# Optimization experiments

Hardware: AMD Instinct MI355X
Metric: run time of the kernel (lower is better)

The kernel has to match this reference:

```python
import jax, jax.numpy as jnp
import numpy as np

N_NODES = 20000
N_EDGES = 320000
N_GRAPHS = 32
C = 256
L = 4
IN_DIM = 739
EDGE_DIM = 2 * C + 6
LN_EPS = 1e-5


def _layernorm(x, g, b):
    mu = jnp.mean(x, axis=-1, keepdims=True)
    var = jnp.mean(jnp.square(x - mu), axis=-1, keepdims=True)
    return (x - mu) * jax.lax.rsqrt(var + LN_EPS) * g + b


def setup_inputs() -> dict:
    key = jax.random.key(0)
    ks = jax.random.split(key, 20)
    d = {}
    d["x"] = jax.random.normal(ks[0], (N_NODES, IN_DIM), jnp.float32)
    d["x_pos"] = jax.random.normal(ks[1], (N_NODES, 3), jnp.float32)
    d["edge_index"] = jax.random.randint(ks[2], (2, N_EDGES), 0, N_NODES, jnp.int32)
    d["batch"] = jnp.sort(jax.random.randint(ks[3], (N_NODES,), 0, N_GRAPHS, jnp.int32))
    s = 0.02
    d["dense_w"] = jax.random.normal(ks[4], (IN_DIM, C), jnp.float32) * s
    d["dense_b"] = jnp.zeros((C,), jnp.float32)
    d["d1_w"] = jax.random.normal(ks[5], (L, C, C), jnp.float32) * s
    d["d1_b"] = jnp.zeros((L, C), jnp.float32)
    d["ln1_g"] = jnp.ones((L, EDGE_DIM), jnp.float32)
    d["ln1_b"] = jnp.zeros((L, EDGE_DIM), jnp.float32)
    d["w1_w"] = jax.random.normal(ks[6], (L, EDGE_DIM, 4), jnp.float32) * s
    d["w1_b"] = jnp.zeros((L, 4), jnp.float32)
    d["ln2_g"] = jnp.ones((L, 4), jnp.float32)
    d["ln2_b"] = jnp.zeros((L, 4), jnp.float32)
    d["w2_w"] = jax.random.normal(ks[7], (L, 4, 1), jnp.float32) * s
    d["w2_b"] = jnp.zeros((L, 1), jnp.float32)
    d["d2_w"] = jax.random.normal(ks[8], (L, C, C), jnp.float32) * s
    d["d2_b"] = jnp.zeros((L, C), jnp.float32)
    d["head_w"] = jax.random.normal(ks[9], (C, 1), jnp.float32) * s
    d["head_b"] = jnp.zeros((1,), jnp.float32)
    return d


def reference(x, x_pos, edge_index, batch, dense_w, dense_b, d1_w, d1_b,
              ln1_g, ln1_b, w1_w, w1_b, ln2_g, ln2_b, w2_w, w2_b,
              d2_w, d2_b, head_w, head_b):
    n = x.shape[0]
    src, dst = edge_index[0], edge_index[1]
    h = x @ dense_w + dense_b  # [N, C]
    for l in range(d1_w.shape[0]):
        # message: dense1 -> GELU (dropout is identity in eval)
        m = jax.nn.gelu(h @ d1_w[l] + d1_b[l], approximate=False)  # [N, C]
        sx = m[src]                                                # [E, C]
        # edge-MLP input: [src_x, dst_x, src_pos, dst_pos]
        e = jnp.concatenate([sx, m[dst], x_pos[src], x_pos[dst]], axis=-1)  # [E, 2C+6]
        e = _layernorm(e, ln1_g[l], ln1_b[l])
        e = jax.nn.gelu(e @ w1_w[l] + w1_b[l], approximate=False)  # [E, 4]
        e = _layernorm(e, ln2_g[l], ln2_b[l])
        w = jax.nn.sigmoid(e @ w2_w[l] + w2_b[l])                  # [E, 1]
        agg = jax.ops.segment_sum(sx * w, dst, num_segments=n)     # [N, C]
        # update: dense2 -> GELU
        h = jax.nn.gelu(agg @ d2_w[l] + d2_b[l], approximate=False)
    # global mean pool over graphs
    sums = jax.ops.segment_sum(h, batch, num_segments=N_GRAPHS)           # [G, C]
    cnts = jax.ops.segment_sum(jnp.ones((n, 1), h.dtype), batch, num_segments=N_GRAPHS)
    pooled = sums / jnp.maximum(cnts, 1.0)
    return pooled @ head_w + head_b  # [G, 1]
```

## Files before the change

### kernel.cpp

```cpp
#include <hip/hip_runtime.h>
#include <math.h>

#define N_NODES 20000
#define N_EDGES 320000
#define N_GRAPHS 32
#define CDIM 256
#define IN_DIMV 739
#define KPAD_DENSE 768
#define ED_DIM 518
#define NLAYERS 4
#define LN_EPS 1e-5f
#define SCAN_BLOCKS ((N_NODES + 255) / 256)

typedef _Float16 f16x8 __attribute__((ext_vector_type(8)));
typedef _Float16 f16x4 __attribute__((ext_vector_type(4)));
typedef float f32x4 __attribute__((ext_vector_type(4)));

__device__ __forceinline__ float gelu_exact(float x) {
    return 0.5f * x * (1.f + erff(x * 0.7071067811865475f));
}

__device__ __forceinline__ void gll16(const void* g, void* l) {
    __builtin_amdgcn_global_load_lds((const __attribute__((address_space(1))) void*)g,
                                     (__attribute__((address_space(3))) void*)l, 16, 0, 0);
}

__global__ __launch_bounds__(256)
void prep_all(const float* __restrict__ ln1_g, const float* __restrict__ ln1_b,
              const float* __restrict__ w1_w, float* __restrict__ cw,
              float* __restrict__ SgSb,
              const float* __restrict__ dense_w, _Float16* __restrict__ wt_dense,
              const float* __restrict__ d1_w, const float* __restrict__ d2_w,
              _Float16* __restrict__ wt_sq, int* __restrict__ deg,
              float* __restrict__ sdot) {
    __shared__ float smem[2048 + 64];
    int b = blockIdx.x, tid = threadIdx.x;
    if (b < 79) {
        int i = b * 256 + tid;
        if (i < N_NODES) deg[i] = 0;
    } else if (b < 83) {
        int l = b - 79;
        float sg[4] = {0, 0, 0, 0}, sb[4] = {0, 0, 0, 0};
        for (int i = tid; i < ED_DIM; i += 256) {
            float g = ln1_g[l * ED_DIM + i];
            float bb = ln1_b[l * ED_DIM + i];
            float4 w = *(const float4*)&w1_w[(size_t)(l * ED_DIM + i) * 4];
            float4 c = make_float4(g * w.x, g * w.y, g * w.z, g * w.w);
            *(float4*)&cw[(size_t)(l * ED_DIM + i) * 4] = c;
            sg[0] += c.x; sg[1] += c.y; sg[2] += c.z; sg[3] += c.w;
            sb[0] += bb * w.x; sb[1] += bb * w.y; sb[2] += bb * w.z; sb[3] += bb * w.w;
        }
        for (int c = 0; c < 4; c++) { smem[tid * 8 + c] = sg[c]; smem[tid * 8 + 4 + c] = sb[c]; }
        __syncthreads();
        for (int s = 128; s > 0; s >>= 1) {
            if (tid < s)
                for (int c = 0; c < 8; c++) smem[tid * 8 + c] += smem[(tid + s) * 8 + c];
            __syncthreads();
        }
        if (tid < 8) SgSb[l * 8 + tid] = smem[tid];
    } else if (b < 275) {
        int q = b - 83;
        int kt = q >> 3, nt = q & 7;
        int i = tid >> 5, j = tid & 31;
        float* T = smem;
#pragma unroll
        for (int ii = 0; ii < 4; ii++) {
            int k = kt * 32 + i + ii * 8;
            T[(i + ii * 8) * 33 + j] = (k < IN_DIMV) ? dense_w[(size_t)k * 256 + nt * 32 + j] : 0.f;
        }
        __syncthreads();
#pragma unroll
        for (int ii = 0; ii < 4; ii++) {
            int n = nt * 32 + i + ii * 8;
            wt_dense[(size_t)n * KPAD_DENSE + kt * 32 + j] = (_Float16)T[j * 33 + i + ii * 8];
        }
    } else if (b < 787) {
        int q = b - 275;
        int z = q >> 6, kt = (q >> 3) & 7, nt = q & 7;
        const float* W = (z < 4) ? d1_w + (size_t)z * 65536 : d2_w + (size_t)(z - 4) * 65536;
        _Float16* O = wt_sq + (size_t)z * 65536;
        int i = tid >> 5, j = tid & 31;
        float* T = smem;
#pragma unroll
        for (int ii = 0; ii < 4; ii++)
            T[(i + ii * 8) * 33 + j] = W[(size_t)(kt * 32 + i + ii * 8) * 256 + nt * 32 + j];
        __syncthreads();
#pragma unroll
        for (int ii = 0; ii < 4; ii++)
            O[(size_t)(nt * 32 + i + ii * 8) * 256 + kt * 32 + j] = (_Float16)T[j * 33 + i + ii * 8];
    } else {
        int i = (b - 787) * 256 + tid;
        if (i < N_NODES) sdot[i] = 0.f;
    }
}

__global__ void hist_gstart_kernel(const int* __restrict__ ei, const int* __restrict__ batch,
                                   int* __restrict__ deg, int* __restrict__ gstart) {
    int e = blockIdx.x * 256 + threadIdx.x;
    if (e < N_EDGES) atomicAdd(&deg[ei[N_EDGES + e]], 1);
    if (e < N_NODES) {
        int b = batch[e];
        int bprev = (e == 0) ? -1 : batch[e - 1];
        for (int g = bprev + 1; g <= b; g++) gstart[g] = e;
        if (e == N_NODES - 1)
            for (int g = b + 1; g <= N_GRAPHS; g++) gstart[g] = N_NODES;
    }
}

__global__ __launch_bounds__(256)
void scan1_kernel(const int* __restrict__ deg, int* __restrict__ bsum) {
    __shared__ int red[256];
    int t = threadIdx.x;
    int i = blockIdx.x * 256 + t;
    red[t] = (i < N_NODES) ? deg[i] : 0;
    __syncthreads();
    for (int s = 128; s > 0; s >>= 1) {
        if (t < s) red[t] += red[t + s];
        __syncthreads();
    }
    if (t == 0) bsum[blockIdx.x] = red[0];
}

__global__ __launch_bounds__(128)
void scan2_kernel(const int* __restrict__ bsum, int* __restrict__ boff) {
    __shared__ int s[128];
    int t = threadIdx.x;
    int v = (t < SCAN_BLOCKS) ? bsum[t] : 0;
    s[t] = v;
    __syncthreads();
    for (int off = 1; off < 128; off <<= 1) {
        int o = (t >= off) ? s[t - off] : 0;
        __syncthreads();
        s[t] += o;
        __syncthreads();
    }
    if (t < SCAN_BLOCKS) boff[t] = s[t] - v;
}

__global__ __launch_bounds__(256)
void scan3_kernel(const int* __restrict__ deg, const int* __restrict__ boff,
                  int* __restrict__ row_start, int* __restrict__ cursor) {
    __shared__ int s[256];
    int t = threadIdx.x;
    int i = blockIdx.x * 256 + t;
    int v = (i < N_NODES) ? deg[i] : 0;
    s[t] = v;
    __syncthreads();
    for (int off = 1; off < 256; off <<= 1) {
        int o = (t >= off) ? s[t - off] : 0;
        __syncthreads();
        s[t] += o;
        __syncthreads();
    }
    int base = boff[blockIdx.x];
    int excl = base + s[t] - v;
    if (i < N_NODES) {
        row_start[i] = excl;
        cursor[i] = excl;
    }
    if (i == N_NODES - 1) row_start[N_NODES] = base + s[t];
}

__global__ void scatter_kernel(const int* __restrict__ ei, int* __restrict__ cursor,
                               int* __restrict__ csr_src, int* __restrict__ slot) {
    int e = blockIdx.x * 256 + threadIdx.x;
    if (e < N_EDGES) {
        int d = ei[N_EDGES + e];
        int pos = atomicAdd(&cursor[d], 1);
        csr_src[pos] = ei[e];
        slot[e] = pos;
    }
}

template <int KSTEPS, int AK, bool AFP32, bool GELU_ACT, bool DOT>
__global__ __launch_bounds__(256)
void gemm_v2(const void* __restrict__ Av, const _Float16* __restrict__ Bt,
             const float* __restrict__ bias, _Float16* __restrict__ C,
             const float* __restrict__ head_w, float* __restrict__ sdot) {
    constexpr int BSTR = KSTEPS * 64;
    __shared__ __align__(16) _Float16 As[2][64 * 64];
    __shared__ __align__(16) _Float16 Bs[2][128 * 64];

    const int tid = threadIdx.x;
    const int row0 = blockIdx.x * 64;
    const int col0 = blockIdx.y * 128;
    const int wave = tid >> 6, lane = tid & 63;
    const int quad = lane >> 4, lrow = lane & 15;
    const int wrow = wave >> 1, wcol = wave & 1;

    const int sr = tid >> 3;
    const int scb = (tid & 7) << 4;
    const int srcCb = scb ^ ((sr & 7) << 4);

    const char* bsrc[4];
#pragma unroll
    for (int i = 0; i < 4; ++i)
        bsrc[i] = (const char*)Bt + (size_t)(col0 + i * 32 + sr) * (BSTR * 2) + srcCb;
    char* const bdst = (char*)&Bs[0][0] + tid * 16;

    const char* asrc[2];
    const float* afsrc[2];
    char* const adst = (char*)&As[0][0] + tid * 16;
    char* const adstw = (char*)&As[0][0] + sr * 128 + srcCb;
#pragma unroll
    for (int i = 0; i < 2; ++i) {
        int ar = row0 + i * 32 + sr;
        ar = (ar < N_NODES) ? ar : (N_NODES - 1);
        asrc[i] = (const char*)Av + (size_t)ar * (AK * 2) + srcCb;
        afsrc[i] = (const float*)Av + (size_t)ar * AK + (scb >> 1);
    }

    const int swz = ((lrow & 7) << 4) ^ (quad << 4);
    const int aro0 = (wrow * 32 + lrow) * 128;
    const int aro1 = aro0 + 2048;
    int bro[4];
#pragma unroll
    for (int t = 0; t < 4; ++t) bro[t] = (wcol * 64 + t * 16 + lrow) * 128;

    f32x4 acc[2][4];
#pragma unroll
    for (int i = 0; i < 2; ++i)
#pragma unroll
        for (int t = 0; t < 4; ++t) acc[i][t] = (f32x4){0.f, 0.f, 0.f, 0.f};

    {
        float av0[8], av1[8];
        if constexpr (AFP32) {
            if constexpr (64 <= AK) {
#pragma unroll
                for (int j = 0; j < 8; ++j) { av0[j] = afsrc[0][j]; av1[j] = afsrc[1][j]; }
            }
        }
#pragma unroll
        for (int i = 0; i < 4; ++i) gll16(bsrc[i], bdst + i * 4096);
        if constexpr (!AFP32) {
#pragma unroll
            for (int i = 0; i < 2; ++i) gll16(asrc[i], adst + i * 4096);
        } else {
            f16x8 v0, v1;
#pragma unroll
            for (int j = 0; j < 8; ++j) { v0[j] = (_Float16)av0[j]; v1[j] = (_Float16)av1[j]; }
            *(f16x8*)(adstw) = v0;
            *(f16x8*)(adstw + 4096) = v1;
        }
    }
    asm volatile("s_waitcnt vmcnt(0)" ::: "memory");
    __syncthreads();

    int cur = 0;
    for (int kt = 0; kt < KSTEPS; ++kt) {
        const bool more = (kt + 1 < KSTEPS);
        float av0[8], av1[8];
        if (more) {
            const int kbyte = (kt + 1) * 128;
            if constexpr (AFP32) {
                const int k0 = (kt + 1) * 64;
                if ((kt + 2) * 64 <= AK) {
#pragma unroll
                    for (int j = 0; j < 8; ++j) { av0[j] = afsrc[0][k0 + j]; av1[j] = afsrc[1][k0 + j]; }
                } else {
                    const int kbase = k0 + (scb >> 1);
#pragma unroll
                    for (int j = 0; j < 8; ++j) {
                        av0[j] = (kbase + j < AK) ? afsrc[0][k0 + j] : 0.f;
                        av1[j] = (kbase + j < AK) ? afsrc[1][k0 + j] : 0.f;
                    }
                }
            }
            const int bb = (cur ^ 1) * 16384;
#pragma unroll
            for (int i = 0; i < 4; ++i) gll16(bsrc[i] + kbyte, bdst + bb + i * 4096);
            if constexpr (!AFP32) {
                const int ab = (cur ^ 1) * 8192;
#pragma unroll
                for (int i = 0; i < 2; ++i) gll16(asrc[i] + kbyte, adst + ab + i * 4096);
            }
        }

        const char* pa = (const char*)&As[0][0] + cur * 8192;
        const char* pb = (const char*)&Bs[0][0] + cur * 16384;
#pragma unroll
        for (int h = 0; h < 2; ++h) {
            const int cbs = (h << 6) ^ swz;
            f16x8 af0 = *(const f16x8*)(pa + aro0 + cbs);
            f16x8 af1 = *(const f16x8*)(pa + aro1 + cbs);
#pragma unroll
            for (int t = 0; t < 4; ++t) {
                f16x8 bf = *(const f16x8*)(pb + bro[t] + cbs);
                acc[0][t] = __builtin_amdgcn_mfma_f32_16x16x32_f16(af0, bf, acc[0][t], 0, 0, 0);
                acc[1][t] = __builtin_amdgcn_mfma_f32_16x16x32_f16(af1, bf, acc[1][t], 0, 0, 0);
            }
        }

        if constexpr (AFP32) {
            if (more) {
                const int ab = (cur ^ 1) * 8192;
                f16x8 v0, v1;
#pragma unroll
                for (int j = 0; j < 8; ++j) { v0[j] = (_Float16)av0[j]; v1[j] = (_Float16)av1[j]; }
                *(f16x8*)(adstw + ab) = v0;
                *(f16x8*)(adstw + ab + 4096) = v1;
            }
        }
        asm volatile("s_waitcnt vmcnt(0)" ::: "memory");
        __syncthreads();
        cur ^= 1;
    }

    const int orow = row0 + wrow * 32 + quad * 4;
    const int ocolb = col0 + wcol * 64 + lrow;
    if constexpr (DOT) {
        float dp0[4] = {0.f, 0.f, 0.f, 0.f}, dp1[4] = {0.f, 0.f, 0.f, 0.f};
#pragma unroll
        for (int t = 0; t < 4; ++t) {
            const int col = ocolb + t * 16;
            const float hw = head_w[col];
            const float bv = bias[col];
#pragma unroll
            for (int r = 0; r < 4; ++r) {
                dp0[r] += gelu_exact(acc[0][t][r] + bv) * hw;
                dp1[r] += gelu_exact(acc[1][t][r] + bv) * hw;
            }
        }
#pragma unroll
        for (int r = 0; r < 4; ++r) {
#pragma unroll
            for (int off = 1; off < 16; off <<= 1) {
                dp0[r] += __shfl_xor(dp0[r], off, 64);
                dp1[r] += __shfl_xor(dp1[r], off, 64);
            }
        }
        if (lrow == 0) {
#pragma unroll
            for (int r = 0; r < 4; ++r) {
                if (orow + r < N_NODES) atomicAdd(&sdot[orow + r], dp0[r]);
                if (orow + 16 + r < N_NODES) atomicAdd(&sdot[orow + 16 + r], dp1[r]);
            }
        }
    } else {
#pragma unroll
        for (int t = 0; t < 4; ++t) {
            const int col = ocolb + t * 16;
            const float bv = bias[col];
#pragma unroll
            for (int r = 0; r < 4; ++r) {
                float v0 = acc[0][t][r] + bv;
                float v1 = acc[1][t][r] + bv;
                if constexpr (GELU_ACT) { v0 = gelu_exact(v0); v1 = gelu_exact(v1); }
                if (orow + r < N_NODES)
                    C[(size_t)(orow + r) * 256 + col] = (_Float16)v0;
                if (orow + 16 + r < N_NODES)
                    C[(size_t)(orow + 16 + r) * 256 + col] = (_Float16)v1;
            }
        }
    }
}

__global__ __launch_bounds__(256)
void node_summary_kernel(const _Float16* __restrict__ m, const float* __restrict__ cw,
                         float* __restrict__ ns) {
    __shared__ __align__(16) float4 s_cw[512];
    int tid = threadIdx.x;
    for (int i = tid; i < 512; i += 256) s_cw[i] = *(const float4*)&cw[(size_t)i * 4];
    __syncthreads();
    int n = blockIdx.x * 4 + (tid >> 6);
    if (n >= N_NODES) return;
    int lane = tid & 63;
    f16x4 a4 = *(const f16x4*)&m[(size_t)n * CDIM + lane * 4];
    float av[4] = {(float)a4[0], (float)a4[1], (float)a4[2], (float)a4[3]};
    float Q1 = 0.f, Q2 = 0.f, P1[4] = {0, 0, 0, 0}, P2[4] = {0, 0, 0, 0};
#pragma unroll
    for (int j = 0; j < 4; j++) {
        Q1 += av[j];
        Q2 += av[j] * av[j];
        float4 c0 = s_cw[lane * 4 + j];
        float4 c1 = s_cw[256 + lane * 4 + j];
        P1[0] += av[j] * c0.x; P1[1] += av[j] * c0.y; P1[2] += av[j] * c0.z; P1[3] += av[j] * c0.w;
        P2[0] += av[j] * c1.x; P2[1] += av[j] * c1.y; P2[2] += av[j] * c1.z; P2[3] += av[j] * c1.w;
    }
#pragma unroll
    for (int off = 1; off < 64; off <<= 1) {
        Q1 += __shfl_xor(Q1, off, 64);
        Q2 += __shfl_xor(Q2, off, 64);
        P1[0] += __shfl_xor(P1[0], off, 64);
        P1[1] += __shfl_xor(P1[1], off, 64);
        P1[2] += __shfl_xor(P1[2], off, 64);
        P1[3] += __shfl_xor(P1[3], off, 64);
        P2[0] += __shfl_xor(P2[0], off, 64);
        P2[1] += __shfl_xor(P2[1], off, 64);
        P2[2] += __shfl_xor(P2[2], off, 64);
        P2[3] += __shfl_xor(P2[3], off, 64);
    }
    if (lane == 0) {
        float* p = &ns[(size_t)n * 12];
        *(float4*)p = make_float4(P1[0], P1[1], P1[2], P1[3]);
        *(float4*)(p + 4) = make_float4(P2[0], P2[1], P2[2], P2[3]);
        p[8] = Q1;
        p[9] = Q2;
    }
}

__global__ __launch_bounds__(256)
void edge_weight_kernel(const float* __restrict__ ns, const float* __restrict__ x_pos,
                        const int* __restrict__ ei, const float* __restrict__ cw,
                        const float* __restrict__ SgSb, const float* __restrict__ w1_b,
                        const float* __restrict__ ln2_g, const float* __restrict__ ln2_b,
                        const float* __restrict__ w2_w, const float* __restrict__ w2_b,
                        const int* __restrict__ slot, float* __restrict__ w_csr) {
    int e = blockIdx.x * 256 + threadIdx.x;
    if (e >= N_EDGES) return;
    int s = ei[e], d = ei[N_EDGES + e];
    const float* nss = &ns[(size_t)s * 12];
    const float* nsd = &ns[(size_t)d * 12];
    float4 p1 = *(const float4*)nss;
    float4 p2 = *(const float4*)(nsd + 4);
    float S1 = nss[8] + nsd[8];
    float S2 = nss[9] + nsd[9];
    float D[4] = {p1.x + p2.x, p1.y + p2.y, p1.z + p2.z, p1.w + p2.w};
    float ps[6];
    ps[0] = x_pos[(size_t)s * 3 + 0];
    ps[1] = x_pos[(size_t)s * 3 + 1];
    ps[2] = x_pos[(size_t)s * 3 + 2];
    ps[3] = x_pos[(size_t)d * 3 + 0];
    ps[4] = x_pos[(size_t)d * 3 + 1];
    ps[5] = x_pos[(size_t)d * 3 + 2];
#pragma unroll
    for (int k = 0; k < 6; k++) {
        S1 += ps[k];
        S2 += ps[k] * ps[k];
        float4 c = *(const float4*)&cw[(size_t)(512 + k) * 4];
        D[0] += ps[k] * c.x; D[1] += ps[k] * c.y; D[2] += ps[k] * c.z; D[3] += ps[k] * c.w;
    }
    const float inv = 1.f / 518.f;
    float mu = S1 * inv;
    float var = fmaf(-mu, mu, S2 * inv);
    float rstd = rsqrtf(var + LN_EPS);
    float t[4];
#pragma unroll
    for (int c = 0; c < 4; c++)
        t[c] = gelu_exact(rstd * (D[c] - mu * SgSb[c]) + SgSb[4 + c] + w1_b[c]);
    float mu2 = 0.25f * (t[0] + t[1] + t[2] + t[3]);
    float var2 = 0.25f * ((t[0] - mu2) * (t[0] - mu2) + (t[1] - mu2) * (t[1] - mu2) +
                          (t[2] - mu2) * (t[2] - mu2) + (t[3] - mu2) * (t[3] - mu2));
    float r2 = rsqrtf(var2 + LN_EPS);
    float z = w2_b[0];
#pragma unroll
    for (int c = 0; c < 4; c++)
        z += ((t[c] - mu2) * r2 * ln2_g[c] + ln2_b[c]) * w2_w[c];
    w_csr[slot[e]] = 1.f / (1.f + expf(-z));
}

__global__ __launch_bounds__(256)
void agg_kernel(const _Float16* __restrict__ m, const int* __restrict__ csr_src,
                const float* __restrict__ w_csr, const int* __restrict__ row_start,
                _Float16* __restrict__ agg) {
    int n = blockIdx.x * 4 + (threadIdx.x >> 6);
    if (n >= N_NODES) return;
    int lane = threadIdx.x & 63;
    int beg = row_start[n], end = row_start[n + 1];
    float a0 = 0.f, a1 = 0.f, a2 = 0.f, a3 = 0.f;
    int j = beg;
    for (; j + 8 <= end; j += 8) {
        int si[8];
        float wi[8];
#pragma unroll
        for (int u = 0; u < 8; u++) { si[u] = csr_src[j + u]; wi[u] = w_csr[j + u]; }
        f16x4 v[8];
#pragma unroll
        for (int u = 0; u < 8; u++) v[u] = *(const f16x4*)&m[(size_t)si[u] * CDIM + lane * 4];
#pragma unroll
        for (int u = 0; u < 8; u++) {
            a0 = fmaf(wi[u], (float)v[u][0], a0);
            a1 = fmaf(wi[u], (float)v[u][1], a1);
            a2 = fmaf(wi[u], (float)v[u][2], a2);
            a3 = fmaf(wi[u], (float)v[u][3], a3);
        }
    }
    for (; j < end; j++) {
        int s = csr_src[j];
        float w = w_csr[j];
        f16x4 v = *(const f16x4*)&m[(size_t)s * CDIM + lane * 4];
        a0 = fmaf(w, (float)v[0], a0);
        a1 = fmaf(w, (float)v[1], a1);
        a2 = fmaf(w, (float)v[2], a2);
        a3 = fmaf(w, (float)v[3], a3);
    }
    f16x4 o;
    o[0] = (_Float16)a0; o[1] = (_Float16)a1; o[2] = (_Float16)a2; o[3] = (_Float16)a3;
    *(f16x4*)&agg[(size_t)n * CDIM + lane * 4] = o;
}

__global__ __launch_bounds__(256)
void final_head_kernel(const float* __restrict__ sdot, const int* __restrict__ gstart,
                       const float* __restrict__ head_b, float* __restrict__ out) {
    int g = blockIdx.x;
    int t = threadIdx.x;
    int beg = gstart[g], end = gstart[g + 1];
    float s = 0.f;
    for (int i = beg + t; i < end; i += 256) s += sdot[i];
    __shared__ float red[256];
    red[t] = s;
    __syncthreads();
    for (int k = 128; k > 0; k >>= 1) {
        if (t < k) red[t] += red[t + k];
        __syncthreads();
    }
    if (t == 0) out[g] = red[0] / fmaxf((float)(end - beg), 1.f) + head_b[0];
}

extern "C" void kernel_launch(void* const* d_in, const int* in_sizes, int n_in,
                              void* d_out, int out_size, void* d_ws, size_t ws_size,
                              hipStream_t stream) {
    const float* x       = (const float*)d_in[0];
    const float* x_pos   = (const float*)d_in[1];
    const int*   ei      = (const int*)d_in[2];
    const int*   batch   = (const int*)d_in[3];
    const float* dense_w = (const float*)d_in[4];
    const float* dense_b = (const float*)d_in[5];
    const float* d1_w    = (const float*)d_in[6];
    const float* d1_b    = (const float*)d_in[7];
    const float* ln1_g   = (const float*)d_in[8];
    const float* ln1_b   = (const float*)d_in[9];
    const float* w1_w    = (const float*)d_in[10];
    const float* w1_b    = (const float*)d_in[11];
    const float* ln2_g   = (const float*)d_in[12];
    const float* ln2_b   = (const float*)d_in[13];
    const float* w2_w    = (const float*)d_in[14];
    const float* w2_b    = (const float*)d_in[15];
    const float* d2_w    = (const float*)d_in[16];
    const float* d2_b    = (const float*)d_in[17];
    const float* head_w  = (const float*)d_in[18];
    const float* head_b  = (const float*)d_in[19];
    float* out = (float*)d_out;

    _Float16* hbuf0 = (_Float16*)d_ws;
    _Float16* hbuf1 = hbuf0 + (size_t)N_NODES * CDIM;
    _Float16* wt_dense = hbuf1 + (size_t)N_NODES * CDIM;
    _Float16* wt_sq    = wt_dense + (size_t)256 * KPAD_DENSE;
    float* cw    = (float*)(wt_sq + (size_t)8 * 256 * 256);
    float* SgSb  = cw + (size_t)NLAYERS * ED_DIM * 4;
    float* ns    = SgSb + NLAYERS * 8;
    float* sdot  = ns + (size_t)N_NODES * 12;
    float* w_csr = sdot + N_NODES;
    int* gstart    = (int*)(w_csr + N_EDGES);
    int* deg       = gstart + N_GRAPHS + 1;
    int* row_start = deg + N_NODES;
    int* cursor    = row_start + N_NODES + 1;
    int* csr_src   = cursor + N_NODES;
    int* slot      = csr_src + N_EDGES;
    int* bsum      = slot + N_EDGES;
    int* boff      = bsum + SCAN_BLOCKS;

    prep_all<<<866, 256, 0, stream>>>(ln1_g, ln1_b, w1_w, cw, SgSb,
                                      dense_w, wt_dense, d1_w, d2_w, wt_sq, deg, sdot);

    hist_gstart_kernel<<<(N_EDGES + 255) / 256, 256, 0, stream>>>(ei, batch, deg, gstart);
    scan1_kernel<<<SCAN_BLOCKS, 256, 0, stream>>>(deg, bsum);
    scan2_kernel<<<1, 128, 0, stream>>>(bsum, boff);
    scan3_kernel<<<SCAN_BLOCKS, 256, 0, stream>>>(deg, boff, row_start, cursor);
    scatter_kernel<<<(N_EDGES + 255) / 256, 256, 0, stream>>>(ei, cursor, csr_src, slot);

    const dim3 G2((N_NODES + 63) / 64, 2);
    gemm_v2<12, IN_DIMV, true, false, false><<<G2, 256, 0, stream>>>(
        x, wt_dense, dense_b, hbuf0, nullptr, nullptr);

    _Float16* h = hbuf0;
    _Float16* other = hbuf1;
    for (int l = 0; l < NLAYERS; l++) {
        gemm_v2<4, CDIM, false, true, false><<<G2, 256, 0, stream>>>(
            h, wt_sq + (size_t)l * 65536, d1_b + l * CDIM, other, nullptr, nullptr);
        node_summary_kernel<<<(N_NODES + 3) / 4, 256, 0, stream>>>(
            other, cw + (size_t)l * ED_DIM * 4, ns);
        edge_weight_kernel<<<(N_EDGES + 255) / 256, 256, 0, stream>>>(
            ns, x_pos, ei, cw + (size_t)l * ED_DIM * 4, SgSb + l * 8, w1_b + l * 4,
            ln2_g + l * 4, ln2_b + l * 4, w2_w + l * 4, w2_b + l, slot, w_csr);
        agg_kernel<<<(N_NODES + 3) / 4, 256, 0, stream>>>(other, csr_src, w_csr, row_start, h);
        if (l < NLAYERS - 1) {
            gemm_v2<4, CDIM, false, true, false><<<G2, 256, 0, stream>>>(
                h, wt_sq + (size_t)(4 + l) * 65536, d2_b + l * CDIM, other, nullptr, nullptr);
        } else {
            gemm_v2<4, CDIM, false, true, true><<<G2, 256, 0, stream>>>(
                h, wt_sq + (size_t)(4 + l) * 65536, d2_b + l * CDIM, other, head_w, sdot);
        }
        _Float16* tmp = h; h = other; other = tmp;
    }

    final_head_kernel<<<N_GRAPHS, 256, 0, stream>>>(sdot, gstart, head_b, out);
}
```

Before: 507.8 us.

## Triple-buffer GEMM shared-memory tiles with explicit waitcnt pipelining and MFMA priority

Restructures the fp16 MFMA GEMM main loop from a double-buffered loop into a fully unrolled three-stage pipeline. It prefetches two K-steps ahead, uses partial vmcnt waits and raw s_barrier instead of draining all loads each step, and raises wave priority around the MFMA block. For fp32 A inputs it keeps double-buffered LDS but double-buffers the register staging. The aim is to hide global-load latency better. In exchange it uses more LDS per block (up to about 72KB), which may lower occupancy, and it relies on hand-tuned waitcnt counts.

```diff
diff --git a/kernel.cpp b/kernel.cpp
--- a/kernel.cpp
+++ b/kernel.cpp
@@ -178,8 +178,8 @@
              const float* __restrict__ bias, _Float16* __restrict__ C,
              const float* __restrict__ head_w, float* __restrict__ sdot) {
     constexpr int BSTR = KSTEPS * 64;
-    __shared__ __align__(16) _Float16 As[2][64 * 64];
-    __shared__ __align__(16) _Float16 Bs[2][128 * 64];
+    __shared__ __align__(16) _Float16 Bs[3 * 128 * 64];
+    __shared__ __align__(16) _Float16 As[(AFP32 ? 2 : 3) * 64 * 64];
 
     const int tid = threadIdx.x;
     const int row0 = blockIdx.x * 64;
@@ -196,12 +196,12 @@
 #pragma unroll
     for (int i = 0; i < 4; ++i)
         bsrc[i] = (const char*)Bt + (size_t)(col0 + i * 32 + sr) * (BSTR * 2) + srcCb;
-    char* const bdst = (char*)&Bs[0][0] + tid * 16;
+    char* const bdst = (char*)&Bs[0] + tid * 16;
 
     const char* asrc[2];
     const float* afsrc[2];
-    char* const adst = (char*)&As[0][0] + tid * 16;
-    char* const adstw = (char*)&As[0][0] + sr * 128 + srcCb;
+    char* const adst = (char*)&As[0] + tid * 16;
+    char* const adstw = (char*)&As[0] + sr * 128 + srcCb;
 #pragma unroll
     for (int i = 0; i < 2; ++i) {
         int ar = row0 + i * 32 + sr;
@@ -223,62 +223,56 @@
 #pragma unroll
         for (int t = 0; t < 4; ++t) acc[i][t] = (f32x4){0.f, 0.f, 0.f, 0.f};
 
-    {
-        float av0[8], av1[8];
+    float av[2][2][8];
+
+    auto stage = [&](int j) {
+        const int kb = j * 128;
+        const int b3 = (j % 3) * 16384;
+#pragma unroll
+        for (int i = 0; i < 4; ++i) gll16(bsrc[i] + kb, bdst + b3 + i * 4096);
+        if constexpr (!AFP32) {
+            const int a3 = (j % 3) * 8192;
+#pragma unroll
+            for (int i = 0; i < 2; ++i) gll16(asrc[i] + kb, adst + a3 + i * 4096);
+        } else {
+            const int k0 = j * 64;
+            const int p = j & 1;
+            if ((j + 1) * 64 <= AK) {
+#pragma unroll
+                for (int jj = 0; jj < 8; ++jj) {
+                    av[p][0][jj] = afsrc[0][k0 + jj];
+                    av[p][1][jj] = afsrc[1][k0 + jj];
+                }
+            } else {
+                const int kbase = k0 + (scb >> 1);
+#pragma unroll
+                for (int jj = 0; jj < 8; ++jj) {
+                    av[p][0][jj] = (kbase + jj < AK) ? afsrc[0][k0 + jj] : 0.f;
+                    av[p][1][jj] = (kbase + jj < AK) ? afsrc[1][k0 + jj] : 0.f;
+                }
+            }
+        }
+    };
+
+    auto awrite = [&](int j) {
         if constexpr (AFP32) {
-            if constexpr (64 <= AK) {
-#pragma unroll
-                for (int j = 0; j < 8; ++j) { av0[j] = afsrc[0][j]; av1[j] = afsrc[1][j]; }
-            }
-        }
-#pragma unroll
-        for (int i = 0; i < 4; ++i) gll16(bsrc[i], bdst + i * 4096);
-        if constexpr (!AFP32) {
-#pragma unroll
-            for (int i = 0; i < 2; ++i) gll16(asrc[i], adst + i * 4096);
-        } else {
+            const int ab = (j & 1) * 8192;
+            const int p = j & 1;
             f16x8 v0, v1;
 #pragma unroll
-            for (int j = 0; j < 8; ++j) { v0[j] = (_Float16)av0[j]; v1[j] = (_Float16)av1[j]; }
-            *(f16x8*)(adstw) = v0;
-            *(f16x8*)(adstw + 4096) = v1;
-        }
-    }
-    asm volatile("s_waitcnt vmcnt(0)" ::: "memory");
-    __syncthreads();
-
-    int cur = 0;
-    for (int kt = 0; kt < KSTEPS; ++kt) {
-        const bool more = (kt + 1 < KSTEPS);
-        float av0[8], av1[8];
-        if (more) {
-            const int kbyte = (kt + 1) * 128;
-            if constexpr (AFP32) {
-                const int k0 = (kt + 1) * 64;
-                if ((kt + 2) * 64 <= AK) {
-#pragma unroll
-                    for (int j = 0; j < 8; ++j) { av0[j] = afsrc[0][k0 + j]; av1[j] = afsrc[1][k0 + j]; }
-                } else {
-                    const int kbase = k0 + (scb >> 1);
-#pragma unroll
-                    for (int j = 0; j < 8; ++j) {
-                        av0[j] = (kbase + j < AK) ? afsrc[0][k0 + j] : 0.f;
-                        av1[j] = (kbase + j < AK) ? afsrc[1][k0 + j] : 0.f;
-                    }
-                }
-            }
-            const int bb = (cur ^ 1) * 16384;
-#pragma unroll
-            for (int i = 0; i < 4; ++i) gll16(bsrc[i] + kbyte, bdst + bb + i * 4096);
-            if constexpr (!AFP32) {
-                const int ab = (cur ^ 1) * 8192;
-#pragma unroll
-                for (int i = 0; i < 2; ++i) gll16(asrc[i] + kbyte, adst + ab + i * 4096);
-            }
-        }
-
-        const char* pa = (const char*)&As[0][0] + cur * 8192;
-        const char* pb = (const char*)&Bs[0][0] + cur * 16384;
+            for (int jj = 0; jj < 8; ++jj) {
+                v0[jj] = (_Float16)av[p][0][jj];
+                v1[jj] = (_Float16)av[p][1][jj];
+            }
+            *(f16x8*)(adstw + ab) = v0;
+            *(f16x8*)(adstw + ab + 4096) = v1;
+        }
+    };
+
+    auto compute = [&](int k) {
+        const char* pa = (const char*)&As[0] + (AFP32 ? (k & 1) : (k % 3)) * 8192;
+        const char* pb = (const char*)&Bs[0] + (k % 3) * 16384;
+        __builtin_amdgcn_s_setprio(1);
 #pragma unroll
         for (int h = 0; h < 2; ++h) {
             const int cbs = (h << 6) ^ swz;
@@ -291,20 +285,46 @@
                 acc[1][t] = __builtin_amdgcn_mfma_f32_16x16x32_f16(af1, bf, acc[1][t], 0, 0, 0);
             }
         }
-
-        if constexpr (AFP32) {
-            if (more) {
-                const int ab = (cur ^ 1) * 8192;
-                f16x8 v0, v1;
-#pragma unroll
-                for (int j = 0; j < 8; ++j) { v0[j] = (_Float16)av0[j]; v1[j] = (_Float16)av1[j]; }
-                *(f16x8*)(adstw + ab) = v0;
-                *(f16x8*)(adstw + ab + 4096) = v1;
-            }
-        }
+        __builtin_amdgcn_s_setprio(0);
+    };
+
+    stage(0);
+    if constexpr (AFP32) {
         asm volatile("s_waitcnt vmcnt(0)" ::: "memory");
-        __syncthreads();
-        cur ^= 1;
+        __builtin_amdgcn_sched_barrier(0);
+        awrite(0);
+        stage(1);
+        asm volatile("s_waitcnt lgkmcnt(0)" ::: "memory");
+    } else {
+        stage(1);
+        asm volatile("s_waitcnt vmcnt(6) lgkmcnt(0)" ::: "memory");
+    }
+    __builtin_amdgcn_sched_barrier(0);
+    __builtin_amdgcn_s_barrier();
+    __builtin_amdgcn_sched_barrier(0);
+
+#pragma unroll
+    for (int k = 0; k < KSTEPS; ++k) {
+        if (k + 2 < KSTEPS) stage(k + 2);
+        compute(k);
+        if (k + 1 < KSTEPS) {
+            if (k + 2 < KSTEPS) {
+                if constexpr (AFP32)
+                    asm volatile("s_waitcnt vmcnt(8) lgkmcnt(0)" ::: "memory");
+                else
+                    asm volatile("s_waitcnt vmcnt(6) lgkmcnt(0)" ::: "memory");
+            } else {
+                asm volatile("s_waitcnt vmcnt(0) lgkmcnt(0)" ::: "memory");
+            }
+            __builtin_amdgcn_sched_barrier(0);
+            if constexpr (AFP32) {
+                awrite(k + 1);
+                asm volatile("s_waitcnt lgkmcnt(0)" ::: "memory");
+                __builtin_amdgcn_sched_barrier(0);
+            }
+            __builtin_amdgcn_s_barrier();
+            __builtin_amdgcn_sched_barrier(0);
+        }
     }
 
     const int orow = row0 + wrow * 32 + quad * 4;
```

Result: slower. 554.5 us (+9.2%).
